# Kernel optimization log

Measured on AMD Instinct MI355X. Metric: run time of the kernel, lower is better.

Reference implementation:

```python
import jax, jax.numpy as jnp
import numpy as np

EMBED_DIM = 2048
NUM_HEADS = 16
LATENT_DIM = 512
HEAD_DIM = EMBED_DIM // NUM_HEADS


def setup_inputs() -> dict:
    key = jax.random.key(0)
    ks = jax.random.split(key, 9)
    s = 0.02
    x = jax.random.normal(ks[0], (2, 2048, EMBED_DIM), dtype=jnp.float32)
    # torch Linear weights stored as [out, in]
    q_w = jax.random.normal(ks[1], (EMBED_DIM, EMBED_DIM), jnp.float32) * s
    q_b = jax.random.normal(ks[2], (EMBED_DIM,), jnp.float32) * s
    kvd_w = jax.random.normal(ks[3], (LATENT_DIM, EMBED_DIM), jnp.float32) * s
    kvd_b = jax.random.normal(ks[4], (LATENT_DIM,), jnp.float32) * s
    kvu_w = jax.random.normal(ks[5], (EMBED_DIM * 2, LATENT_DIM), jnp.float32) * s
    kvu_b = jax.random.normal(ks[6], (EMBED_DIM * 2,), jnp.float32) * s
    out_w = jax.random.normal(ks[7], (EMBED_DIM, EMBED_DIM), jnp.float32) * s
    out_b = jax.random.normal(ks[8], (EMBED_DIM,), jnp.float32) * s
    return {"x": x, "q_w": q_w, "q_b": q_b, "kvd_w": kvd_w, "kvd_b": kvd_b,
            "kvu_w": kvu_w, "kvu_b": kvu_b, "out_w": out_w, "out_b": out_b}


def reference(x, q_w, q_b, kvd_w, kvd_b, kvu_w, kvu_b, out_w, out_b):
    b, s, _ = x.shape
    q = x @ q_w.T + q_b                      # [b,s,E]
    latent = x @ kvd_w.T + kvd_b             # [b,s,L]
    kv = latent @ kvu_w.T + kvu_b            # [b,s,2E]
    k, v = kv[..., :EMBED_DIM], kv[..., EMBED_DIM:]
    def heads(t):
        return t.reshape(b, s, NUM_HEADS, HEAD_DIM).transpose(0, 2, 1, 3)  # [b,h,s,d]
    qh, kh, vh = heads(q), heads(k), heads(v)
    scores = jnp.einsum('bhqd,bhkd->bhqk', qh, kh) / jnp.sqrt(jnp.float32(HEAD_DIM))
    attn = jax.nn.softmax(scores, axis=-1)
    out = jnp.einsum('bhqk,bhkd->bhqd', attn, vh)
    out = out.transpose(0, 2, 1, 3).reshape(b, s, EMBED_DIM)
    return out @ out_w.T + out_b
```

## Files before the change

kernel.cpp:

```cpp
#include <hip/hip_runtime.h>

typedef unsigned short u16;
typedef __attribute__((ext_vector_type(8))) __bf16 bf16x8;
typedef __attribute__((ext_vector_type(8))) unsigned short u16x8;
typedef __attribute__((ext_vector_type(4))) float f32x4;
typedef __attribute__((ext_vector_type(16))) float f32x16;

#define BK 32
#define TILE_ELEMS (128 * BK)
#define QSCALE 0.12753706518066536f

#if __has_builtin(__builtin_amdgcn_exp2f)
#define EXP2(x) __builtin_amdgcn_exp2f(x)
#else
#define EXP2(x) exp2f(x)
#endif

__device__ __forceinline__ u16 f32_to_bf16(float f) {
  __bf16 h = (__bf16)f;
  return __builtin_bit_cast(u16, h);
}

__device__ __forceinline__ void gll16(const u16* g, u16* l) {
  __builtin_amdgcn_global_load_lds(
      (const __attribute__((address_space(1))) void*)g,
      (__attribute__((address_space(3))) void*)l, 16, 0, 0);
}

__device__ __forceinline__ void xcd_swz(int& bn, int& bm) {
  const int nx = gridDim.x;
  const int nwg = nx * gridDim.y;
  const int wg = blockIdx.y * nx + blockIdx.x;
  const int cpx = nwg >> 3;
  const int swz = (wg & 7) * cpx + (wg >> 3);
  bn = swz % nx;
  bm = swz / nx;
}

__global__ __launch_bounds__(256) void cvt_all(
    const float* __restrict__ x, const float* __restrict__ qw,
    const float* __restrict__ kvdw, const float* __restrict__ kvuw,
    const float* __restrict__ outw, u16* __restrict__ X, u16* __restrict__ W1,
    u16* __restrict__ W2, u16* __restrict__ W3, u16* __restrict__ W4) {
  int blk = blockIdx.x;
  const float* src;
  u16* dst;
  int base;
  if (blk < 8192)       { src = x;    dst = X;  base = blk; }
  else if (blk < 12288) { src = qw;   dst = W1; base = blk - 8192; }
  else if (blk < 13312) { src = kvdw; dst = W2; base = blk - 12288; }
  else if (blk < 15360) { src = kvuw; dst = W3; base = blk - 13312; }
  else                  { src = outw; dst = W4; base = blk - 15360; }
  int i = base * 1024 + threadIdx.x * 4;
  float4 v = *(const float4*)(src + i);
  ushort4 o;
  o.x = f32_to_bf16(v.x);
  o.y = f32_to_bf16(v.y);
  o.z = f32_to_bf16(v.z);
  o.w = f32_to_bf16(v.w);
  *(ushort4*)(dst + i) = o;
}

__device__ __forceinline__ void gemm_core(const u16* __restrict__ A_tile,
                                          const u16* __restrict__ B_tile, int K,
                                          u16* As, u16* Bs, f32x4 acc[4][4]) {
  const int tid = threadIdx.x;
  const int w = tid >> 6, lane = tid & 63;
  const int wm = (w >> 1) << 6, wn = (w & 1) << 6;
  const int quad = lane >> 4, l15 = lane & 15;

  const u16* Ap = A_tile + (tid >> 2) * K + (tid & 3) * 8;
  const u16* Bp = B_tile + (tid >> 2) * K + (tid & 3) * 8;
  u16* Asw = As + w * 512;
  u16* Bsw = Bs + w * 512;

  gll16(Ap, Asw);
  gll16(Ap + 64 * K, Asw + 2048);
  gll16(Bp, Bsw);
  gll16(Bp + 64 * K, Bsw + 2048);

  int p = 0;
  for (int k0 = 0; k0 < K; k0 += BK) {
    const int kn = k0 + BK;
    __syncthreads();
    if (kn < K) {
      const int off = (p ^ 1) * TILE_ELEMS;
      gll16(Ap + kn, Asw + off);
      gll16(Ap + 64 * K + kn, Asw + off + 2048);
      gll16(Bp + kn, Bsw + off);
      gll16(Bp + 64 * K + kn, Bsw + off + 2048);
    }
    const u16* Asr = As + p * TILE_ELEMS;
    const u16* Bsr = Bs + p * TILE_ELEMS;
    bf16x8 af[4], bf[4];
#pragma unroll
    for (int i = 0; i < 4; i++)
      af[i] = *(const bf16x8*)(Asr + (wm + i * 16 + l15) * BK + quad * 8);
#pragma unroll
    for (int j = 0; j < 4; j++)
      bf[j] = *(const bf16x8*)(Bsr + (wn + j * 16 + l15) * BK + quad * 8);
#pragma unroll
    for (int i = 0; i < 4; i++)
#pragma unroll
      for (int j = 0; j < 4; j++)
        acc[i][j] =
            __builtin_amdgcn_mfma_f32_16x16x32_bf16(af[i], bf[j], acc[i][j], 0, 0, 0);
    p ^= 1;
  }
}

__global__ __launch_bounds__(256) void gemm_qlat(const u16* __restrict__ X,
                                                 const u16* __restrict__ QW,
                                                 const u16* __restrict__ KVDW,
                                                 const float* __restrict__ q_b,
                                                 const float* __restrict__ kvd_b,
                                                 u16* __restrict__ Qb,
                                                 u16* __restrict__ Lat) {
  __shared__ __align__(16) u16 As[2 * TILE_ELEMS];
  __shared__ __align__(16) u16 Bs[2 * TILE_ELEMS];
  int bn, bm;
  xcd_swz(bn, bm);
  const bool isq = bn < 16;
  const u16* B_tile = isq ? QW + (size_t)bn * 128 * 2048
                          : KVDW + (size_t)(bn - 16) * 128 * 2048;
  f32x4 acc[4][4];
  const f32x4 z = {0.f, 0.f, 0.f, 0.f};
#pragma unroll
  for (int i = 0; i < 4; i++)
#pragma unroll
    for (int j = 0; j < 4; j++) acc[i][j] = z;
  gemm_core(X + (size_t)bm * 128 * 2048, B_tile, 2048, As, Bs, acc);

  const float* bias = isq ? q_b : kvd_b;
  u16* C = isq ? Qb : Lat;
  const int N = isq ? 2048 : 512;
  const float scale = isq ? QSCALE : 1.0f;
  const int colbase = (isq ? bn : bn - 16) * 128;

  const int tid = threadIdx.x;
  const int w = tid >> 6, lane = tid & 63;
  const int wm = (w >> 1) << 6, wn = (w & 1) << 6;
  const int quad = lane >> 4, l15 = lane & 15;
  const int row0 = bm * 128 + wm + quad * 4;
  const int col0 = colbase + wn + l15;
#pragma unroll
  for (int i = 0; i < 4; i++)
#pragma unroll
    for (int j = 0; j < 4; j++) {
      int col = col0 + j * 16;
      float bv = bias[col];
#pragma unroll
      for (int r = 0; r < 4; r++) {
        int row = row0 + i * 16 + r;
        C[(size_t)row * N + col] = f32_to_bf16((acc[i][j][r] + bv) * scale);
      }
    }
}

__global__ __launch_bounds__(256) void gemm_f32out(const u16* __restrict__ A,
                                                   const u16* __restrict__ B,
                                                   const float* __restrict__ bias,
                                                   float* __restrict__ C, int K, int N) {
  __shared__ __align__(16) u16 As[2 * TILE_ELEMS];
  __shared__ __align__(16) u16 Bs[2 * TILE_ELEMS];
  int bn, bm;
  xcd_swz(bn, bm);
  f32x4 acc[4][4];
  const f32x4 z = {0.f, 0.f, 0.f, 0.f};
#pragma unroll
  for (int i = 0; i < 4; i++)
#pragma unroll
    for (int j = 0; j < 4; j++) acc[i][j] = z;
  gemm_core(A + (size_t)bm * 128 * K, B + (size_t)bn * 128 * K, K, As, Bs, acc);

  const int tid = threadIdx.x;
  const int w = tid >> 6, lane = tid & 63;
  const int wm = (w >> 1) << 6, wn = (w & 1) << 6;
  const int quad = lane >> 4, l15 = lane & 15;
  const int row0 = bm * 128 + wm + quad * 4;
  const int col0 = bn * 128 + wn + l15;
#pragma unroll
  for (int i = 0; i < 4; i++)
#pragma unroll
    for (int j = 0; j < 4; j++) {
      int col = col0 + j * 16;
      float bv = bias[col];
#pragma unroll
      for (int r = 0; r < 4; r++) {
        int row = row0 + i * 16 + r;
        C[(size_t)row * N + col] = acc[i][j][r] + bv;
      }
    }
}

__global__ __launch_bounds__(256) void gemm_kv(const u16* __restrict__ A,
                                               const u16* __restrict__ B,
                                               const float* __restrict__ bias,
                                               u16* __restrict__ Khat,
                                               u16* __restrict__ Vt, int K) {
  __shared__ __align__(16) u16 As[2 * TILE_ELEMS];
  __shared__ __align__(16) u16 Bs[2 * TILE_ELEMS];
  int bn, bm;
  xcd_swz(bn, bm);
  f32x4 acc[4][4];
  const f32x4 z = {0.f, 0.f, 0.f, 0.f};
#pragma unroll
  for (int i = 0; i < 4; i++)
#pragma unroll
    for (int j = 0; j < 4; j++) acc[i][j] = z;
  gemm_core(A + (size_t)bm * 128 * K, B + (size_t)bn * 128 * K, K, As, Bs, acc);

  const int tid = threadIdx.x;
  const int w = tid >> 6, lane = tid & 63;
  const int wm = (w >> 1) << 6, wn = (w & 1) << 6;
  const int quad = lane >> 4, l15 = lane & 15;
  const int row0 = bm * 128 + wm + quad * 4;
  const int col0 = bn * 128 + wn + l15;
#pragma unroll
  for (int i = 0; i < 4; i++)
#pragma unroll
    for (int j = 0; j < 4; j++) {
      int n = col0 + j * 16;
      float bv = bias[n];
#pragma unroll
      for (int r = 0; r < 4; r++) {
        int row = row0 + i * 16 + r;
        int bb = row >> 11, s = row & 2047;
        u16 val = f32_to_bf16(acc[i][j][r] + bv);
        if (n < 2048) {
          int h = n >> 7, d = n & 127;
          Khat[((size_t)(bb * 16 + h) * 2048 + s) * 128 + d] = val;
        } else {
          int h = (n - 2048) >> 7, d = n & 127;
          Vt[((size_t)(bb * 16 + h) * 128 + d) * 2048 + s] = val;
        }
      }
    }
}

__global__ __launch_bounds__(256) void attn_kernel(const u16* __restrict__ Q,
                                                   const u16* __restrict__ Khat,
                                                   const u16* __restrict__ Vt,
                                                   u16* __restrict__ O) {
  __shared__ __align__(16) u16 Ks[2][32 * 136];
  __shared__ __align__(16) u16 Vs[2][128 * 40];

  const int tid = threadIdx.x;
  const int w = tid >> 6, lane = tid & 63;
  const int l31 = lane & 31, half = lane >> 5;
  const int idx = blockIdx.x;
  const int swz = (idx & 7) * 64 + (idx >> 3);
  const int qt = swz & 15;
  const int h = (swz >> 4) & 15;
  const int b = swz >> 8;
  const int bh = b * 16 + h;

  bf16x8 qf[8];
  {
    const u16* qrow = Q + (size_t)(b * 2048 + qt * 128 + w * 32 + l31) * 2048 +
                      h * 128 + half * 8;
#pragma unroll
    for (int kc = 0; kc < 8; kc++) qf[kc] = *(const bf16x8*)(qrow + kc * 16);
  }

  f32x16 oacc[4];
#pragma unroll
  for (int nt = 0; nt < 4; nt++)
#pragma unroll
    for (int r = 0; r < 16; r++) oacc[nt][r] = 0.f;
  float ls0 = 0.f, ls1 = 0.f, ls2 = 0.f, ls3 = 0.f;

  const u16* Kg = Khat + (size_t)bh * 2048 * 128;
  const u16* Vg = Vt + (size_t)bh * 128 * 2048;

  const int kkr = tid >> 4, kc0 = tid & 15;
  const int vd = tid >> 2, vc0 = tid & 3;
  const int vlo = (vc0 >> 1) * 16 + (vc0 & 1) * 4;
  const int vhi = vlo + 8;

  u16x8 kv[2], vv[2];
#pragma unroll
  for (int it = 0; it < 2; it++) {
    kv[it] = *(const u16x8*)(Kg + (size_t)(kkr + it * 16) * 128 + kc0 * 8);
    vv[it] = *(const u16x8*)(Vg + (size_t)(vd + it * 64) * 2048 + vc0 * 8);
  }
#pragma unroll
  for (int it = 0; it < 2; it++) {
    *(u16x8*)(Ks[0] + (kkr + it * 16) * 136 + kc0 * 8) = kv[it];
    const unsigned long long* vp = (const unsigned long long*)&vv[it];
    *(unsigned long long*)(Vs[0] + (vd + it * 64) * 40 + vlo) = vp[0];
    *(unsigned long long*)(Vs[0] + (vd + it * 64) * 40 + vhi) = vp[1];
  }

  int p = 0;
  for (int key0 = 0; key0 < 2048; key0 += 32) {
    const int kn = (key0 + 32 < 2048) ? (key0 + 32) : 0;
#pragma unroll
    for (int it = 0; it < 2; it++) {
      kv[it] = *(const u16x8*)(Kg + (size_t)(kn + kkr + it * 16) * 128 + kc0 * 8);
      vv[it] = *(const u16x8*)(Vg + (size_t)(vd + it * 64) * 2048 + kn + vc0 * 8);
    }
    __syncthreads();

    f32x16 sacc;
#pragma unroll
    for (int r = 0; r < 16; r++) sacc[r] = 0.f;
    __builtin_amdgcn_s_setprio(1);
#pragma unroll
    for (int kc = 0; kc < 8; kc++) {
      bf16x8 kf = *(const bf16x8*)(Ks[p] + l31 * 136 + kc * 16 + half * 8);
      sacc = __builtin_amdgcn_mfma_f32_32x32x16_bf16(kf, qf[kc], sacc, 0, 0, 0);
    }
    __builtin_amdgcn_s_setprio(0);

    float e[16];
#pragma unroll
    for (int r = 0; r < 16; r++) e[r] = EXP2(sacc[r]);
    ls0 += e[0] + e[4] + e[8] + e[12];
    ls1 += e[1] + e[5] + e[9] + e[13];
    ls2 += e[2] + e[6] + e[10] + e[14];
    ls3 += e[3] + e[7] + e[11] + e[15];
    bf16x8 pa0, pa1;
#pragma unroll
    for (int i = 0; i < 8; i++) {
      pa0[i] = (__bf16)e[i];
      pa1[i] = (__bf16)e[8 + i];
    }

    __builtin_amdgcn_s_setprio(1);
#pragma unroll
    for (int nt = 0; nt < 4; nt++) {
      bf16x8 vf0 = *(const bf16x8*)(Vs[p] + (nt * 32 + l31) * 40 + half * 8);
      bf16x8 vf1 = *(const bf16x8*)(Vs[p] + (nt * 32 + l31) * 40 + 16 + half * 8);
      oacc[nt] = __builtin_amdgcn_mfma_f32_32x32x16_bf16(pa0, vf0, oacc[nt], 0, 0, 0);
      oacc[nt] = __builtin_amdgcn_mfma_f32_32x32x16_bf16(pa1, vf1, oacc[nt], 0, 0, 0);
    }
    __builtin_amdgcn_s_setprio(0);

    const int pn = p ^ 1;
#pragma unroll
    for (int it = 0; it < 2; it++) {
      *(u16x8*)(Ks[pn] + (kkr + it * 16) * 136 + kc0 * 8) = kv[it];
      const unsigned long long* vp = (const unsigned long long*)&vv[it];
      *(unsigned long long*)(Vs[pn] + (vd + it * 64) * 40 + vlo) = vp[0];
      *(unsigned long long*)(Vs[pn] + (vd + it * 64) * 40 + vhi) = vp[1];
    }
    p = pn;
  }

  float lsum = (ls0 + ls1) + (ls2 + ls3);
  lsum += __shfl_xor(lsum, 32);
  float inv = 1.0f / lsum;
  float wr[16];
#pragma unroll
  for (int r = 0; r < 16; r++) {
    int ridx = (r & 3) + 8 * (r >> 2) + 4 * half;
    wr[r] = __shfl(inv, ridx);
  }

#pragma unroll
  for (int nt = 0; nt < 4; nt++)
#pragma unroll
    for (int r = 0; r < 16; r++) {
      int ridx = (r & 3) + 8 * (r >> 2) + 4 * half;
      int row = b * 2048 + qt * 128 + w * 32 + ridx;
      int col = h * 128 + nt * 32 + l31;
      O[(size_t)row * 2048 + col] = f32_to_bf16(oacc[nt][r] * wr[r]);
    }
}

extern "C" void kernel_launch(void* const* d_in, const int* in_sizes, int n_in,
                              void* d_out, int out_size, void* d_ws, size_t ws_size,
                              hipStream_t stream) {
  (void)in_sizes; (void)n_in; (void)out_size; (void)ws_size;
  const float* x     = (const float*)d_in[0];
  const float* q_w   = (const float*)d_in[1];
  const float* q_b   = (const float*)d_in[2];
  const float* kvd_w = (const float*)d_in[3];
  const float* kvd_b = (const float*)d_in[4];
  const float* kvu_w = (const float*)d_in[5];
  const float* kvu_b = (const float*)d_in[6];
  const float* out_w = (const float*)d_in[7];
  const float* out_b = (const float*)d_in[8];
  float* out = (float*)d_out;

  char* p = (char*)d_ws;
  u16* X    = (u16*)(p + 0);
  u16* W1   = (u16*)(p + (size_t)16 * 1024 * 1024);
  u16* W2   = (u16*)(p + (size_t)24 * 1024 * 1024);
  u16* W3   = (u16*)(p + (size_t)26 * 1024 * 1024);
  u16* W4   = (u16*)(p + (size_t)30 * 1024 * 1024);
  u16* Qb   = (u16*)(p + (size_t)38 * 1024 * 1024);
  u16* Lat  = (u16*)(p + (size_t)54 * 1024 * 1024);
  u16* Khat = (u16*)(p + (size_t)58 * 1024 * 1024);
  u16* Vt   = (u16*)(p + (size_t)74 * 1024 * 1024);
  u16* AO   = (u16*)(p + (size_t)90 * 1024 * 1024);

  cvt_all<<<dim3(19456), dim3(256), 0, stream>>>(x, q_w, kvd_w, kvu_w, out_w,
                                                 X, W1, W2, W3, W4);
  gemm_qlat<<<dim3(20, 32), dim3(256), 0, stream>>>(X, W1, W2, q_b, kvd_b, Qb, Lat);
  gemm_kv<<<dim3(32, 32), dim3(256), 0, stream>>>(Lat, W3, kvu_b, Khat, Vt, 512);
  attn_kernel<<<dim3(512), dim3(256), 0, stream>>>(Qb, Khat, Vt, AO);
  gemm_f32out<<<dim3(16, 32), dim3(256), 0, stream>>>(AO, W4, out_b, out, 2048, 2048);
}
```

Before: 362.0 us.

## Load attention K/V fragments directly from global memory, dropping LDS staging

Removes the shared-memory double-buffered K/V tiles and __syncthreads in the attention loop. Each wave now loads its own K and V MFMA fragments straight from global into registers, software-pipelining K with two register sets (ka/kb). This removes LDS writes, reads and barriers. In exchange, all 4 waves of a block redundantly fetch the same K/V data from global/L2, V loads become narrow 8-byte strided accesses, and register pressure rises.

```diff
diff --git a/kernel.cpp b/kernel.cpp
--- a/kernel.cpp
+++ b/kernel.cpp
@@ -1,6 +1,7 @@
 #include <hip/hip_runtime.h>
 
 typedef unsigned short u16;
+typedef __attribute__((ext_vector_type(4))) unsigned short u16x4;
 typedef __attribute__((ext_vector_type(8))) __bf16 bf16x8;
 typedef __attribute__((ext_vector_type(8))) unsigned short u16x8;
 typedef __attribute__((ext_vector_type(4))) float f32x4;
@@ -238,13 +239,63 @@
     }
 }
 
+__device__ __forceinline__ void attn_loadK(const u16* __restrict__ Kg, int key0,
+                                           int l31, int half, bf16x8* kf) {
+  const u16* krow = Kg + (size_t)(key0 + l31) * 128 + half * 8;
+#pragma unroll
+  for (int kc = 0; kc < 8; kc++) kf[kc] = *(const bf16x8*)(krow + kc * 16);
+}
+
+__device__ __forceinline__ void attn_tile32(const u16* __restrict__ Vg,
+                                            const bf16x8* qf, const bf16x8* kf,
+                                            int key0, int l31, int half,
+                                            f32x16* oacc, float* ls) {
+  bf16x8 vf0[4], vf1[4];
+#pragma unroll
+  for (int nt = 0; nt < 4; nt++) {
+    const u16* vrow = Vg + (size_t)(nt * 32 + l31) * 2048 + key0 + 4 * half;
+    *(u16x4*)&vf0[nt] = *(const u16x4*)(vrow);
+    *((u16x4*)&vf0[nt] + 1) = *(const u16x4*)(vrow + 8);
+    *(u16x4*)&vf1[nt] = *(const u16x4*)(vrow + 16);
+    *((u16x4*)&vf1[nt] + 1) = *(const u16x4*)(vrow + 24);
+  }
+
+  f32x16 sacc;
+#pragma unroll
+  for (int r = 0; r < 16; r++) sacc[r] = 0.f;
+  __builtin_amdgcn_s_setprio(1);
+#pragma unroll
+  for (int kc = 0; kc < 8; kc++)
+    sacc = __builtin_amdgcn_mfma_f32_32x32x16_bf16(kf[kc], qf[kc], sacc, 0, 0, 0);
+  __builtin_amdgcn_s_setprio(0);
+
+  float e[16];
+#pragma unroll
+  for (int r = 0; r < 16; r++) e[r] = EXP2(sacc[r]);
+  ls[0] += e[0] + e[4] + e[8] + e[12];
+  ls[1] += e[1] + e[5] + e[9] + e[13];
+  ls[2] += e[2] + e[6] + e[10] + e[14];
+  ls[3] += e[3] + e[7] + e[11] + e[15];
+  bf16x8 pa0, pa1;
+#pragma unroll
+  for (int i = 0; i < 8; i++) {
+    pa0[i] = (__bf16)e[i];
+    pa1[i] = (__bf16)e[8 + i];
+  }
+
+  __builtin_amdgcn_s_setprio(1);
+#pragma unroll
+  for (int nt = 0; nt < 4; nt++) {
+    oacc[nt] = __builtin_amdgcn_mfma_f32_32x32x16_bf16(pa0, vf0[nt], oacc[nt], 0, 0, 0);
+    oacc[nt] = __builtin_amdgcn_mfma_f32_32x32x16_bf16(pa1, vf1[nt], oacc[nt], 0, 0, 0);
+  }
+  __builtin_amdgcn_s_setprio(0);
+}
+
 __global__ __launch_bounds__(256) void attn_kernel(const u16* __restrict__ Q,
                                                    const u16* __restrict__ Khat,
                                                    const u16* __restrict__ Vt,
                                                    u16* __restrict__ O) {
-  __shared__ __align__(16) u16 Ks[2][32 * 136];
-  __shared__ __align__(16) u16 Vs[2][128 * 40];
-
   const int tid = threadIdx.x;
   const int w = tid >> 6, lane = tid & 63;
   const int l31 = lane & 31, half = lane >> 5;
@@ -268,87 +319,21 @@
   for (int nt = 0; nt < 4; nt++)
 #pragma unroll
     for (int r = 0; r < 16; r++) oacc[nt][r] = 0.f;
-  float ls0 = 0.f, ls1 = 0.f, ls2 = 0.f, ls3 = 0.f;
+  float ls[4] = {0.f, 0.f, 0.f, 0.f};
 
   const u16* Kg = Khat + (size_t)bh * 2048 * 128;
   const u16* Vg = Vt + (size_t)bh * 128 * 2048;
 
-  const int kkr = tid >> 4, kc0 = tid & 15;
-  const int vd = tid >> 2, vc0 = tid & 3;
-  const int vlo = (vc0 >> 1) * 16 + (vc0 & 1) * 4;
-  const int vhi = vlo + 8;
-
-  u16x8 kv[2], vv[2];
-#pragma unroll
-  for (int it = 0; it < 2; it++) {
-    kv[it] = *(const u16x8*)(Kg + (size_t)(kkr + it * 16) * 128 + kc0 * 8);
-    vv[it] = *(const u16x8*)(Vg + (size_t)(vd + it * 64) * 2048 + vc0 * 8);
-  }
-#pragma unroll
-  for (int it = 0; it < 2; it++) {
-    *(u16x8*)(Ks[0] + (kkr + it * 16) * 136 + kc0 * 8) = kv[it];
-    const unsigned long long* vp = (const unsigned long long*)&vv[it];
-    *(unsigned long long*)(Vs[0] + (vd + it * 64) * 40 + vlo) = vp[0];
-    *(unsigned long long*)(Vs[0] + (vd + it * 64) * 40 + vhi) = vp[1];
-  }
-
-  int p = 0;
-  for (int key0 = 0; key0 < 2048; key0 += 32) {
-    const int kn = (key0 + 32 < 2048) ? (key0 + 32) : 0;
-#pragma unroll
-    for (int it = 0; it < 2; it++) {
-      kv[it] = *(const u16x8*)(Kg + (size_t)(kn + kkr + it * 16) * 128 + kc0 * 8);
-      vv[it] = *(const u16x8*)(Vg + (size_t)(vd + it * 64) * 2048 + kn + vc0 * 8);
-    }
-    __syncthreads();
-
-    f32x16 sacc;
-#pragma unroll
-    for (int r = 0; r < 16; r++) sacc[r] = 0.f;
-    __builtin_amdgcn_s_setprio(1);
-#pragma unroll
-    for (int kc = 0; kc < 8; kc++) {
-      bf16x8 kf = *(const bf16x8*)(Ks[p] + l31 * 136 + kc * 16 + half * 8);
-      sacc = __builtin_amdgcn_mfma_f32_32x32x16_bf16(kf, qf[kc], sacc, 0, 0, 0);
-    }
-    __builtin_amdgcn_s_setprio(0);
-
-    float e[16];
-#pragma unroll
-    for (int r = 0; r < 16; r++) e[r] = EXP2(sacc[r]);
-    ls0 += e[0] + e[4] + e[8] + e[12];
-    ls1 += e[1] + e[5] + e[9] + e[13];
-    ls2 += e[2] + e[6] + e[10] + e[14];
-    ls3 += e[3] + e[7] + e[11] + e[15];
-    bf16x8 pa0, pa1;
-#pragma unroll
-    for (int i = 0; i < 8; i++) {
-      pa0[i] = (__bf16)e[i];
-      pa1[i] = (__bf16)e[8 + i];
-    }
-
-    __builtin_amdgcn_s_setprio(1);
-#pragma unroll
-    for (int nt = 0; nt < 4; nt++) {
-      bf16x8 vf0 = *(const bf16x8*)(Vs[p] + (nt * 32 + l31) * 40 + half * 8);
-      bf16x8 vf1 = *(const bf16x8*)(Vs[p] + (nt * 32 + l31) * 40 + 16 + half * 8);
-      oacc[nt] = __builtin_amdgcn_mfma_f32_32x32x16_bf16(pa0, vf0, oacc[nt], 0, 0, 0);
-      oacc[nt] = __builtin_amdgcn_mfma_f32_32x32x16_bf16(pa1, vf1, oacc[nt], 0, 0, 0);
-    }
-    __builtin_amdgcn_s_setprio(0);
-
-    const int pn = p ^ 1;
-#pragma unroll
-    for (int it = 0; it < 2; it++) {
-      *(u16x8*)(Ks[pn] + (kkr + it * 16) * 136 + kc0 * 8) = kv[it];
-      const unsigned long long* vp = (const unsigned long long*)&vv[it];
-      *(unsigned long long*)(Vs[pn] + (vd + it * 64) * 40 + vlo) = vp[0];
-      *(unsigned long long*)(Vs[pn] + (vd + it * 64) * 40 + vhi) = vp[1];
-    }
-    p = pn;
-  }
-
-  float lsum = (ls0 + ls1) + (ls2 + ls3);
+  bf16x8 ka[8], kb[8];
+  attn_loadK(Kg, 0, l31, half, ka);
+  for (int key0 = 0; key0 < 2048; key0 += 64) {
+    attn_loadK(Kg, key0 + 32, l31, half, kb);
+    attn_tile32(Vg, qf, ka, key0, l31, half, oacc, ls);
+    if (key0 + 64 < 2048) attn_loadK(Kg, key0 + 64, l31, half, ka);
+    attn_tile32(Vg, qf, kb, key0 + 32, l31, half, oacc, ls);
+  }
+
+  float lsum = (ls[0] + ls[1]) + (ls[2] + ls[3]);
   lsum += __shfl_xor(lsum, 32);
   float inv = 1.0f / lsum;
   float wr[16];
```

After: 622.4 us. 71.9% more time.

## Split attention head dim across wave pairs with 512-thread blocks

Applied to the files above, without the earlier changes.

Doubles the attention block to 8 waves. Each pair of waves shares a 32-row query group and splits the 128-wide head dimension of the PV product in half, so each wave holds half the output accumulators. This cuts per-wave register pressure and adds parallelism, and each thread now loads one K/V chunk instead of two. The cost is that the QK^T scores and exp are computed twice, once by each wave in the pair.

```diff
diff --git a/kernel.cpp b/kernel.cpp
--- a/kernel.cpp
+++ b/kernel.cpp
@@ -238,16 +238,17 @@
     }
 }
 
-__global__ __launch_bounds__(256) void attn_kernel(const u16* __restrict__ Q,
-                                                   const u16* __restrict__ Khat,
-                                                   const u16* __restrict__ Vt,
-                                                   u16* __restrict__ O) {
+__global__ __launch_bounds__(512, 4) void attn_kernel(const u16* __restrict__ Q,
+                                                      const u16* __restrict__ Khat,
+                                                      const u16* __restrict__ Vt,
+                                                      u16* __restrict__ O) {
   __shared__ __align__(16) u16 Ks[2][32 * 136];
   __shared__ __align__(16) u16 Vs[2][128 * 40];
 
   const int tid = threadIdx.x;
   const int w = tid >> 6, lane = tid & 63;
   const int l31 = lane & 31, half = lane >> 5;
+  const int qg = w >> 1, dh = w & 1;
   const int idx = blockIdx.x;
   const int swz = (idx & 7) * 64 + (idx >> 3);
   const int qt = swz & 15;
@@ -257,15 +258,15 @@
 
   bf16x8 qf[8];
   {
-    const u16* qrow = Q + (size_t)(b * 2048 + qt * 128 + w * 32 + l31) * 2048 +
+    const u16* qrow = Q + (size_t)(b * 2048 + qt * 128 + qg * 32 + l31) * 2048 +
                       h * 128 + half * 8;
 #pragma unroll
     for (int kc = 0; kc < 8; kc++) qf[kc] = *(const bf16x8*)(qrow + kc * 16);
   }
 
-  f32x16 oacc[4];
-#pragma unroll
-  for (int nt = 0; nt < 4; nt++)
+  f32x16 oacc[2];
+#pragma unroll
+  for (int nt = 0; nt < 2; nt++)
 #pragma unroll
     for (int r = 0; r < 16; r++) oacc[nt][r] = 0.f;
   float ls0 = 0.f, ls1 = 0.f, ls2 = 0.f, ls3 = 0.f;
@@ -278,28 +279,21 @@
   const int vlo = (vc0 >> 1) * 16 + (vc0 & 1) * 4;
   const int vhi = vlo + 8;
 
-  u16x8 kv[2], vv[2];
-#pragma unroll
-  for (int it = 0; it < 2; it++) {
-    kv[it] = *(const u16x8*)(Kg + (size_t)(kkr + it * 16) * 128 + kc0 * 8);
-    vv[it] = *(const u16x8*)(Vg + (size_t)(vd + it * 64) * 2048 + vc0 * 8);
-  }
-#pragma unroll
-  for (int it = 0; it < 2; it++) {
-    *(u16x8*)(Ks[0] + (kkr + it * 16) * 136 + kc0 * 8) = kv[it];
-    const unsigned long long* vp = (const unsigned long long*)&vv[it];
-    *(unsigned long long*)(Vs[0] + (vd + it * 64) * 40 + vlo) = vp[0];
-    *(unsigned long long*)(Vs[0] + (vd + it * 64) * 40 + vhi) = vp[1];
+  u16x8 kv, vv;
+  kv = *(const u16x8*)(Kg + (size_t)kkr * 128 + kc0 * 8);
+  vv = *(const u16x8*)(Vg + (size_t)vd * 2048 + vc0 * 8);
+  {
+    *(u16x8*)(Ks[0] + kkr * 136 + kc0 * 8) = kv;
+    const unsigned long long* vp = (const unsigned long long*)&vv;
+    *(unsigned long long*)(Vs[0] + vd * 40 + vlo) = vp[0];
+    *(unsigned long long*)(Vs[0] + vd * 40 + vhi) = vp[1];
   }
 
   int p = 0;
   for (int key0 = 0; key0 < 2048; key0 += 32) {
     const int kn = (key0 + 32 < 2048) ? (key0 + 32) : 0;
-#pragma unroll
-    for (int it = 0; it < 2; it++) {
-      kv[it] = *(const u16x8*)(Kg + (size_t)(kn + kkr + it * 16) * 128 + kc0 * 8);
-      vv[it] = *(const u16x8*)(Vg + (size_t)(vd + it * 64) * 2048 + kn + vc0 * 8);
-    }
+    kv = *(const u16x8*)(Kg + (size_t)(kn + kkr) * 128 + kc0 * 8);
+    vv = *(const u16x8*)(Vg + (size_t)vd * 2048 + kn + vc0 * 8);
     __syncthreads();
 
     f32x16 sacc;
@@ -329,21 +323,21 @@
 
     __builtin_amdgcn_s_setprio(1);
 #pragma unroll
-    for (int nt = 0; nt < 4; nt++) {
+    for (int nt2 = 0; nt2 < 2; nt2++) {
+      const int nt = dh * 2 + nt2;
       bf16x8 vf0 = *(const bf16x8*)(Vs[p] + (nt * 32 + l31) * 40 + half * 8);
       bf16x8 vf1 = *(const bf16x8*)(Vs[p] + (nt * 32 + l31) * 40 + 16 + half * 8);
-      oacc[nt] = __builtin_amdgcn_mfma_f32_32x32x16_bf16(pa0, vf0, oacc[nt], 0, 0, 0);
-      oacc[nt] = __builtin_amdgcn_mfma_f32_32x32x16_bf16(pa1, vf1, oacc[nt], 0, 0, 0);
+      oacc[nt2] = __builtin_amdgcn_mfma_f32_32x32x16_bf16(pa0, vf0, oacc[nt2], 0, 0, 0);
+      oacc[nt2] = __builtin_amdgcn_mfma_f32_32x32x16_bf16(pa1, vf1, oacc[nt2], 0, 0, 0);
     }
     __builtin_amdgcn_s_setprio(0);
 
     const int pn = p ^ 1;
-#pragma unroll
-    for (int it = 0; it < 2; it++) {
-      *(u16x8*)(Ks[pn] + (kkr + it * 16) * 136 + kc0 * 8) = kv[it];
-      const unsigned long long* vp = (const unsigned long long*)&vv[it];
-      *(unsigned long long*)(Vs[pn] + (vd + it * 64) * 40 + vlo) = vp[0];
-      *(unsigned long long*)(Vs[pn] + (vd + it * 64) * 40 + vhi) = vp[1];
+    {
+      *(u16x8*)(Ks[pn] + kkr * 136 + kc0 * 8) = kv;
+      const unsigned long long* vp = (const unsigned long long*)&vv;
+      *(unsigned long long*)(Vs[pn] + vd * 40 + vlo) = vp[0];
+      *(unsigned long long*)(Vs[pn] + vd * 40 + vhi) = vp[1];
     }
     p = pn;
   }
@@ -359,13 +353,13 @@
   }
 
 #pragma unroll
-  for (int nt = 0; nt < 4; nt++)
+  for (int nt2 = 0; nt2 < 2; nt2++)
 #pragma unroll
     for (int r = 0; r < 16; r++) {
       int ridx = (r & 3) + 8 * (r >> 2) + 4 * half;
-      int row = b * 2048 + qt * 128 + w * 32 + ridx;
-      int col = h * 128 + nt * 32 + l31;
-      O[(size_t)row * 2048 + col] = f32_to_bf16(oacc[nt][r] * wr[r]);
+      int row = b * 2048 + qt * 128 + qg * 32 + ridx;
+      int col = h * 128 + (dh * 2 + nt2) * 32 + l31;
+      O[(size_t)row * 2048 + col] = f32_to_bf16(oacc[nt2][r] * wr[r]);
     }
 }
 
@@ -400,6 +394,6 @@
                                                  X, W1, W2, W3, W4);
   gemm_qlat<<<dim3(20, 32), dim3(256), 0, stream>>>(X, W1, W2, q_b, kvd_b, Qb, Lat);
   gemm_kv<<<dim3(32, 32), dim3(256), 0, stream>>>(Lat, W3, kvu_b, Khat, Vt, 512);
-  attn_kernel<<<dim3(512), dim3(256), 0, stream>>>(Qb, Khat, Vt, AO);
+  attn_kernel<<<dim3(512), dim3(512), 0, stream>>>(Qb, Khat, Vt, AO);
   gemm_f32out<<<dim3(16, 32), dim3(256), 0, stream>>>(AO, W4, out_b, out, 2048, 2048);
 }
```

After: 384.8 us. 6.3% more time.
